# Kernel tuning notes

Hardware: AMD Instinct MI355X
Metric: run time of the kernel (lower is better)

## Reference

```python
import jax, jax.numpy as jnp
import numpy as np
import math

N, B, S = 2048, 4, 1024
SFZ, IFZ, H, A = 384, 256, 8, 64
LN_EPS = 1e-5


def setup_inputs() -> dict:
    key = jax.random.key(0)
    ks = jax.random.split(key, 12)
    x = jax.random.normal(ks[0], (N, IFZ), dtype=jnp.float32)
    emb = jax.random.normal(ks[1], (B, S, SFZ), dtype=jnp.float32)
    mask = jax.random.randint(ks[2], (B, S), 0, 2).astype(bool)
    batch = jnp.sort(jax.random.randint(ks[3], (N,), 0, B)).astype(jnp.int64)
    sc = 1.0 / math.sqrt(IFZ)
    scs = 1.0 / math.sqrt(SFZ)
    Wq = jax.random.normal(ks[4], (IFZ, H * A), dtype=jnp.float32) * sc
    Wk = jax.random.normal(ks[5], (SFZ, H * A), dtype=jnp.float32) * scs
    Wv = jax.random.normal(ks[6], (SFZ, H * A), dtype=jnp.float32) * scs
    Wg = jax.random.normal(ks[7], (IFZ, H * A), dtype=jnp.float32) * sc
    bg = jnp.zeros((H * A,), dtype=jnp.float32)
    Wback = jax.random.normal(ks[8], (H * A, IFZ), dtype=jnp.float32) / math.sqrt(H * A)
    bback = jnp.zeros((IFZ,), dtype=jnp.float32)
    gamma = jnp.ones((IFZ,), dtype=jnp.float32)
    beta = jnp.zeros((IFZ,), dtype=jnp.float32)
    return {"x": x, "packed_sequence_emb": emb, "packed_sequence_mask": mask,
            "batch": batch, "Wq": Wq, "Wk": Wk, "Wv": Wv, "Wg": Wg, "bg": bg,
            "Wback": Wback, "bback": bback, "gamma": gamma, "beta": beta}


def _masked_softmax(scores, mask):
    # scores: [N,S,H], mask: [N,S,1] bool; softmax over S with padded entries zeroed
    neg = jnp.finfo(scores.dtype).min
    s = jnp.where(mask, scores, neg)
    s = s - jnp.max(s, axis=1, keepdims=True)
    e = jnp.exp(s) * mask
    return e / (jnp.sum(e, axis=1, keepdims=True) + 1e-9)


def reference(x, packed_sequence_emb, packed_sequence_mask, batch,
              Wq, Wk, Wv, Wg, bg, Wback, bback, gamma, beta):
    scale = math.sqrt(A)
    q = (x @ Wq).reshape(N, H, A)                               # [N,H,A]
    k = (packed_sequence_emb @ Wk).reshape(B, S, H, A)          # [B,S,H,A]
    v = (packed_sequence_emb @ Wv).reshape(B, S, H, A)
    # scores per (node, candidate-batch), then gather node's own batch entry;
    # avoids materializing k[batch] of shape [N,S,H,A]
    scores_all = jnp.einsum('nha,bsha->nbsh', q, k) / scale     # [N,B,S,H]
    idx = batch[:, None, None, None].astype(jnp.int32)
    scores = jnp.take_along_axis(scores_all, idx, axis=1)[:, 0]  # [N,S,H]
    bmask = packed_sequence_mask[batch][..., None]               # [N,S,1]
    w = _masked_softmax(scores, bmask)                           # [N,S,H]
    feat_all = jnp.einsum('nsh,bsha->nbha', w, v)                # [N,B,H,A]
    feat = jnp.take_along_axis(feat_all, idx, axis=1)[:, 0]      # [N,H,A]
    gate = jax.nn.sigmoid(x @ Wg + bg).reshape(N, H, A)
    new = (gate * feat).reshape(N, H * A) @ Wback + bback        # [N,IFZ]
    y = math.sqrt(2.0) * x + new
    mu = jnp.mean(y, axis=-1, keepdims=True)
    var = jnp.mean((y - mu) ** 2, axis=-1, keepdims=True)
    out = (y - mu) * jax.lax.rsqrt(var + LN_EPS) * gamma + beta
    seq_aa_logits = jnp.sum(scores[..., :2], axis=-1)            # [N,S]
    return out, seq_aa_logits
```

## Files before the change

### kernel.cpp

```cpp
#include <hip/hip_runtime.h>
#include <hip/hip_bf16.h>

#define NND 2048
#define BBATCH 4
#define SS 1024
#define SFZ 384
#define IFZ 256
#define HH 8
#define AA 64
#define HA 512
#define ABLK 12
#define NGRP 4
#define NSPL 8
#define ATTN_BLKS (BBATCH * ABLK * 16)
#define LOGIT_BLKS (BBATCH * ABLK * 2)

typedef __attribute__((ext_vector_type(8))) short bf16x8;
typedef __attribute__((ext_vector_type(4))) float f32x4;
typedef __attribute__((ext_vector_type(2))) unsigned int u32x2;

__device__ __forceinline__ unsigned short f2bf(float f) {
    union { float f; unsigned u; } a; a.f = f;
    unsigned r = a.u + 0x7fffu + ((a.u >> 16) & 1u);
    return (unsigned short)(r >> 16);
}
__device__ __forceinline__ float bf2f(unsigned short u) {
    return __uint_as_float((unsigned)u << 16);
}

__device__ __forceinline__ bf16x8 cvt8(const float* __restrict__ p) {
    const float4 f0 = *(const float4*)p;
    const float4 f1 = *(const float4*)(p + 4);
    bf16x8 o;
    o[0] = (short)f2bf(f0.x); o[1] = (short)f2bf(f0.y);
    o[2] = (short)f2bf(f0.z); o[3] = (short)f2bf(f0.w);
    o[4] = (short)f2bf(f1.x); o[5] = (short)f2bf(f1.y);
    o[6] = (short)f2bf(f1.z); o[7] = (short)f2bf(f1.w);
    return o;
}

__device__ __forceinline__ bf16x8 gld16(const unsigned short* p) {
    bf16x8 r;
    asm volatile("global_load_dwordx4 %0, %1, off" : "=&v"(r) : "v"(p));
    return r;
}
__device__ __forceinline__ f32x4 gldf4(const float* p) {
    f32x4 r;
    asm volatile("global_load_dwordx4 %0, %1, off" : "=&v"(r) : "v"(p));
    return r;
}
__device__ __forceinline__ u32x2 gld8(const unsigned short* p) {
    u32x2 r;
    asm volatile("global_load_dwordx2 %0, %1, off" : "=&v"(r) : "v"(p));
    return r;
}
#define VMWAIT0() do { \
    asm volatile("s_waitcnt vmcnt(0)" ::: "memory"); \
    __builtin_amdgcn_sched_barrier(0); \
} while (0)

__device__ __forceinline__ void tile_transpose(
    const float* __restrict__ src, unsigned short* __restrict__ dst,
    int K, int N, int kt, int nt, int t)
{
    __shared__ unsigned short tile[64][65];
    const int k0 = kt * 64, n0 = nt * 64;
    const int tr = t >> 6, tc = t & 63;
    #pragma unroll
    for (int r = 0; r < 16; ++r)
        tile[tr + r*4][tc] = f2bf(src[(size_t)(k0 + tr + r*4) * N + n0 + tc]);
    __syncthreads();
    #pragma unroll
    for (int r = 0; r < 16; ++r)
        dst[(size_t)(n0 + tr + r*4) * K + k0 + tc] = tile[tc][tr + r*4];
}

__global__ __launch_bounds__(256) void prep_kernel(
    const float* __restrict__ Wk, const float* __restrict__ Wv,
    const float* __restrict__ Wq, const float* __restrict__ Wg,
    const float* __restrict__ Wback,
    const void* __restrict__ mask_raw, const void* __restrict__ batch_raw,
    unsigned short* __restrict__ WkT, unsigned short* __restrict__ WvT,
    unsigned short* __restrict__ WqT, unsigned short* __restrict__ WgT,
    unsigned short* __restrict__ WbackT,
    float* __restrict__ mask_f, int* __restrict__ seg)
{
    const int bx = blockIdx.x, t = threadIdx.x;
    if (bx < 48)  { tile_transpose(Wk, WkT, SFZ, HA, bx/8, bx%8, t); return; }
    if (bx < 96)  { const int i = bx-48;  tile_transpose(Wv, WvT, SFZ, HA, i/8, i%8, t); return; }
    if (bx < 128) { const int i = bx-96;  tile_transpose(Wq, WqT, IFZ, HA, i/8, i%8, t); return; }
    if (bx < 160) { const int i = bx-128; tile_transpose(Wg, WgT, IFZ, HA, i/8, i%8, t); return; }
    if (bx < 192) { const int i = bx-160; tile_transpose(Wback, WbackT, HA, IFZ, i/4, i%4, t); return; }
    __shared__ int fl[4];
    __shared__ int fb;
    __shared__ int cnt[4];
    if (t < 4) { fl[t] = 0; cnt[t] = 0; }
    if (t == 0) fb = 0;
    __syncthreads();
    const unsigned char*  mb = (const unsigned char*)mask_raw;
    const unsigned short* mh = (const unsigned short*)mask_raw;
    const unsigned int*   mw = (const unsigned int*)mask_raw;
    int f0 = 0, f1 = 0, f2 = 0, f3 = 0;
    for (int i = t; i < 2048; i += 256) {
        unsigned short h = mh[i];
        if (h == 0x3f80u) f0 = 1;
        if ((i & 1) == 0 && h != 0) f1 = 1;
    }
    for (int i = t; i < 4096; i += 256)
        if ((i & 3) != 0 && mb[i] != 0) f2 = 1;
    for (int i = t; i < 1024; i += 256)
        if ((i & 1) != 0 && mw[i] != 0) f3 = 1;
    const int* bw = (const int*)batch_raw;
    int f4 = 0;
    for (int i = t + 1; i < 2048; i += 256)
        if (bw[i] < bw[i-1]) f4 = 1;
    if (f0) atomicOr(&fl[0], 1);
    if (f1) atomicOr(&fl[1], 1);
    if (f2) atomicOr(&fl[2], 1);
    if (f3) atomicOr(&fl[3], 1);
    if (f4) atomicOr(&fb, 1);
    __syncthreads();
    int mode;
    if (fl[0])      mode = fl[1] ? 1 : 0;
    else if (fl[2]) mode = 2;
    else if (fl[3]) mode = 3;
    else            mode = 4;
    for (int s = t; s < BBATCH*SS; s += 256) {
        int m;
        switch (mode) {
            case 0:  m = (mw[s]   != 0); break;
            case 1:  m = (mh[s]   != 0); break;
            case 2:  m = (mb[s]   != 0); break;
            case 3:  m = (mw[s]   != 0); break;
            default: m = (mw[2*s] != 0); break;
        }
        mask_f[s] = m ? 1.0f : 0.0f;
    }
    const int b64 = fb;
    for (int i = t; i < NND; i += 256) {
        const int bv = (b64 ? bw[2*i] : bw[i]) & 3;
        atomicAdd(&cnt[bv], 1);
    }
    __syncthreads();
    if (t == 0) {
        int s = 0;
        for (int b = 0; b < 4; ++b) { seg[2*b] = s; s += cnt[b]; seg[2*b+1] = s; }
    }
}

__global__ __launch_bounds__(256, 2) void proj_mfma(
    const float* __restrict__ emb, const float* __restrict__ x,
    const unsigned short* __restrict__ WkT, const unsigned short* __restrict__ WvT,
    const unsigned short* __restrict__ WqT, const unsigned short* __restrict__ WgT,
    const float* __restrict__ bg,
    unsigned short* __restrict__ k_blk, unsigned short* __restrict__ vT_bf,
    unsigned short* __restrict__ q_bf, float* __restrict__ gate_ws)
{
    __shared__ unsigned short v_l[16][520];
    const int t = threadIdx.x, w = t >> 6, lane = t & 63;
    const int m16 = lane & 15, quad = lane >> 4;
    const int bx = blockIdx.x;
    if (bx < 256) {
        const int r0 = bx * 16;
        const int b = r0 >> 10, srow = r0 & (SS - 1);
        const float* ap = emb + (size_t)(r0 + m16) * SFZ + quad * 8;
        bf16x8 af[12];
        #pragma unroll
        for (int j = 0; j < 12; ++j) af[j] = cvt8(ap + j * 32);
        #pragma unroll
        for (int tensor = 0; tensor < 2; ++tensor) {
            const unsigned short* Wt = tensor ? WvT : WkT;
            #pragma unroll
            for (int g = 0; g < 2; ++g) {
                const int n0g = w * 128 + g * 64;
                const unsigned short* bp0 = Wt + (size_t)(n0g +  0 + m16) * SFZ + quad * 8;
                const unsigned short* bp1 = Wt + (size_t)(n0g + 16 + m16) * SFZ + quad * 8;
                const unsigned short* bp2 = Wt + (size_t)(n0g + 32 + m16) * SFZ + quad * 8;
                const unsigned short* bp3 = Wt + (size_t)(n0g + 48 + m16) * SFZ + quad * 8;
                f32x4 a0 = (f32x4){0.f, 0.f, 0.f, 0.f};
                f32x4 a1 = a0, a2 = a0, a3 = a0;
                bf16x8 wb[24];
                #pragma unroll
                for (int j = 0; j < 6; ++j) {
                    wb[j*4+0] = gld16(bp0 + j * 32);
                    wb[j*4+1] = gld16(bp1 + j * 32);
                    wb[j*4+2] = gld16(bp2 + j * 32);
                    wb[j*4+3] = gld16(bp3 + j * 32);
                }
                VMWAIT0();
                #pragma unroll
                for (int j = 0; j < 6; ++j) {
                    a0 = __builtin_amdgcn_mfma_f32_16x16x32_bf16(af[j], wb[j*4+0], a0, 0, 0, 0);
                    a1 = __builtin_amdgcn_mfma_f32_16x16x32_bf16(af[j], wb[j*4+1], a1, 0, 0, 0);
                    a2 = __builtin_amdgcn_mfma_f32_16x16x32_bf16(af[j], wb[j*4+2], a2, 0, 0, 0);
                    a3 = __builtin_amdgcn_mfma_f32_16x16x32_bf16(af[j], wb[j*4+3], a3, 0, 0, 0);
                }
                #pragma unroll
                for (int j = 6; j < 12; ++j) {
                    wb[(j-6)*4+0] = gld16(bp0 + j * 32);
                    wb[(j-6)*4+1] = gld16(bp1 + j * 32);
                    wb[(j-6)*4+2] = gld16(bp2 + j * 32);
                    wb[(j-6)*4+3] = gld16(bp3 + j * 32);
                }
                VMWAIT0();
                #pragma unroll
                for (int j = 6; j < 12; ++j) {
                    a0 = __builtin_amdgcn_mfma_f32_16x16x32_bf16(af[j], wb[(j-6)*4+0], a0, 0, 0, 0);
                    a1 = __builtin_amdgcn_mfma_f32_16x16x32_bf16(af[j], wb[(j-6)*4+1], a1, 0, 0, 0);
                    a2 = __builtin_amdgcn_mfma_f32_16x16x32_bf16(af[j], wb[(j-6)*4+2], a2, 0, 0, 0);
                    a3 = __builtin_amdgcn_mfma_f32_16x16x32_bf16(af[j], wb[(j-6)*4+3], a3, 0, 0, 0);
                }
                f32x4 dd[4] = {a0, a1, a2, a3};
                if (tensor == 0) {
                    #pragma unroll
                    for (int u = 0; u < 4; ++u) {
                        const int n0 = n0g + u * 16;
                        const int head = n0 >> 6, coff = (n0 & 63) + m16;
                        unsigned short* kb = k_blk + (((size_t)(b * HH + head)) * SS) * 64 + coff;
                        #pragma unroll
                        for (int r = 0; r < 4; ++r)
                            kb[(size_t)(srow + quad * 4 + r) * 64] = f2bf(dd[u][r]);
                    }
                } else {
                    #pragma unroll
                    for (int u = 0; u < 4; ++u) {
                        const int c0 = n0g + u * 16 + m16;
                        #pragma unroll
                        for (int r = 0; r < 4; ++r)
                            v_l[quad * 4 + r][c0] = f2bf(dd[u][r]);
                    }
                }
            }
        }
        __syncthreads();
        for (int c = t; c < HA; c += 256) {
            unsigned short tmp[16];
            #pragma unroll
            for (int s = 0; s < 16; ++s) tmp[s] = v_l[s][c];
            unsigned short* dst = vT_bf + ((size_t)b * HA + c) * SS + srow;
            *(uint4*)dst       = ((const uint4*)tmp)[0];
            *(uint4*)(dst + 8) = ((const uint4*)tmp)[1];
        }
    } else {
        const int i = bx - 256;
        const int r0 = (i >> 1) * 16;
        const int half = i & 1;
        const float* ap = x + (size_t)(r0 + m16) * IFZ + quad * 8;
        bf16x8 af[8];
        #pragma unroll
        for (int j = 0; j < 8; ++j) af[j] = cvt8(ap + j * 32);
        const int n0b = half * 256 + w * 64;
        #pragma unroll
        for (int tensor = 0; tensor < 2; ++tensor) {
            const unsigned short* Wt = tensor ? WgT : WqT;
            const unsigned short* bp0 = Wt + (size_t)(n0b +  0 + m16) * IFZ + quad * 8;
            const unsigned short* bp1 = Wt + (size_t)(n0b + 16 + m16) * IFZ + quad * 8;
            const unsigned short* bp2 = Wt + (size_t)(n0b + 32 + m16) * IFZ + quad * 8;
            const unsigned short* bp3 = Wt + (size_t)(n0b + 48 + m16) * IFZ + quad * 8;
            bf16x8 wb[32];
            #pragma unroll
            for (int j = 0; j < 8; ++j) {
                wb[j*4+0] = gld16(bp0 + j * 32);
                wb[j*4+1] = gld16(bp1 + j * 32);
                wb[j*4+2] = gld16(bp2 + j * 32);
                wb[j*4+3] = gld16(bp3 + j * 32);
            }
            VMWAIT0();
            f32x4 a0 = (f32x4){0.f, 0.f, 0.f, 0.f};
            f32x4 a1 = a0, a2 = a0, a3 = a0;
            #pragma unroll
            for (int j = 0; j < 8; ++j) {
                a0 = __builtin_amdgcn_mfma_f32_16x16x32_bf16(af[j], wb[j*4+0], a0, 0, 0, 0);
                a1 = __builtin_amdgcn_mfma_f32_16x16x32_bf16(af[j], wb[j*4+1], a1, 0, 0, 0);
                a2 = __builtin_amdgcn_mfma_f32_16x16x32_bf16(af[j], wb[j*4+2], a2, 0, 0, 0);
                a3 = __builtin_amdgcn_mfma_f32_16x16x32_bf16(af[j], wb[j*4+3], a3, 0, 0, 0);
            }
            f32x4 dd[4] = {a0, a1, a2, a3};
            if (tensor == 0) {
                #pragma unroll
                for (int u = 0; u < 4; ++u) {
                    const int n0 = n0b + u * 16;
                    #pragma unroll
                    for (int r = 0; r < 4; ++r)
                        q_bf[(size_t)(r0 + quad * 4 + r) * HA + n0 + m16] = f2bf(dd[u][r]);
                }
            } else {
                #pragma unroll
                for (int u = 0; u < 4; ++u) {
                    const int n0 = n0b + u * 16;
                    const float bgv = bg[n0 + m16];
                    #pragma unroll
                    for (int r = 0; r < 4; ++r)
                        gate_ws[(size_t)(r0 + quad * 4 + r) * HA + n0 + m16] =
                            1.f / (1.f + __expf(-(dd[u][r] + bgv)));
                }
            }
        }
    }
}

__global__ __launch_bounds__(256, 2) void attn_kernel(
    const unsigned short* __restrict__ k_blk, const unsigned short* __restrict__ vT_bf,
    const unsigned short* __restrict__ q_bf, const float* __restrict__ mask_f,
    const int* __restrict__ seg, unsigned short* __restrict__ part_O,
    float2* __restrict__ part_ml, float* __restrict__ out_logits)
{
    __shared__ unsigned short P_lds[4][16][136];
    const int bid = blockIdx.x;
    const int t = threadIdx.x;
    const int w = t >> 6, lane = t & 63;
    const int m16 = lane & 15, quad = lane >> 4;

    if (bid >= ATTN_BLKS) {
        const int lid = bid - ATTN_BLKS;
        const int b = lid / 24;
        const int rem = lid % 24;
        const int xblk = rem >> 1;
        const int spair = rem & 1;
        const int s0 = (spair * 4 + w) * 128;
        const int nbase = seg[2*b] + xblk * 64;
        const int nend  = seg[2*b + 1];
        if (nbase >= nend) return;
        const unsigned short* kb0 = k_blk + ((size_t)(b * HH + 0)) * SS * 64;
        const unsigned short* kb1 = k_blk + ((size_t)(b * HH + 1)) * SS * 64;
        bf16x8 k0[16], k1[16];
        #pragma unroll
        for (int st = 0; st < 8; ++st) {
            const unsigned short* kp0 = kb0 + (size_t)(s0 + st * 16 + m16) * 64 + quad * 8;
            const unsigned short* kp1 = kb1 + (size_t)(s0 + st * 16 + m16) * 64 + quad * 8;
            k0[2*st]   = gld16(kp0);
            k0[2*st+1] = gld16(kp0 + 32);
            k1[2*st]   = gld16(kp1);
            k1[2*st+1] = gld16(kp1 + 32);
        }
        VMWAIT0();
        for (int g = 0; g < NGRP; ++g) {
            const int n0g = nbase + g * 16;
            if (n0g >= nend) break;
            const int nvalid = min(16, nend - n0g);
            int nq = n0g + m16; if (nq >= nend) nq = nend - 1;
            const unsigned short* qp = q_bf + (size_t)nq * HA + quad * 8;
            const bf16x8 q0a = gld16(qp);
            const bf16x8 q0b = gld16(qp + 32);
            const bf16x8 q1a = gld16(qp + 64);
            const bf16x8 q1b = gld16(qp + 96);
            VMWAIT0();
            #pragma unroll
            for (int st = 0; st < 8; ++st) {
                f32x4 acc = (f32x4){0.f, 0.f, 0.f, 0.f};
                acc = __builtin_amdgcn_mfma_f32_16x16x32_bf16(q0a, k0[2*st],   acc, 0, 0, 0);
                acc = __builtin_amdgcn_mfma_f32_16x16x32_bf16(q0b, k0[2*st+1], acc, 0, 0, 0);
                acc = __builtin_amdgcn_mfma_f32_16x16x32_bf16(q1a, k1[2*st],   acc, 0, 0, 0);
                acc = __builtin_amdgcn_mfma_f32_16x16x32_bf16(q1b, k1[2*st+1], acc, 0, 0, 0);
                #pragma unroll
                for (int r = 0; r < 4; ++r) {
                    const int row = quad * 4 + r;
                    if (row < nvalid)
                        out_logits[(size_t)(n0g + row) * SS + s0 + st * 16 + m16] =
                            acc[r] * 0.125f;
                }
            }
        }
        return;
    }

    const int xcd = bid & 7;
    const int b   = xcd >> 1;
    const int idx = (bid >> 3) * 2 + (xcd & 1);
    const int z    = idx & 15;
    const int xblk = idx >> 4;
    const int hz    = z >> 3;
    const int split = z & 7;
    const int nbase = seg[2*b] + xblk * (16 * NGRP);
    const int nend  = seg[2*b + 1];
    if (nbase >= nend) return;

    const int h = hz * 4 + w;
    const int s0 = split * 128;

    const unsigned short* kb = k_blk + ((size_t)(b * HH + h)) * SS * 64;
    const unsigned short* vb = vT_bf + ((size_t)b * HA + h * AA) * SS;
    const unsigned short* qbase = q_bf + (size_t)h * AA + quad * 8;
    unsigned short (*Pw)[136] = P_lds[w];

    bf16x8 kf[16];
    #pragma unroll
    for (int st = 0; st < 8; ++st) {
        const unsigned short* kp = kb + (size_t)(s0 + st * 16 + m16) * 64 + quad * 8;
        kf[2*st]   = gld16(kp);
        kf[2*st+1] = gld16(kp + 32);
    }
    f32x4 mkv[8];
    #pragma unroll
    for (int st = 0; st < 8; ++st)
        mkv[st] = gldf4(mask_f + b * SS + s0 + st * 16 + quad * 4);
    int nq0 = nbase + m16; if (nq0 >= nend) nq0 = nend - 1;
    bf16x8 qc0 = gld16(qbase + (size_t)nq0 * HA);
    bf16x8 qc1 = gld16(qbase + (size_t)nq0 * HA + 32);
    VMWAIT0();
    unsigned bm = 0u;
    #pragma unroll
    for (int st = 0; st < 8; ++st)
        #pragma unroll
        for (int r = 0; r < 4; ++r)
            if (mkv[st][r] > 0.5f) bm |= (1u << (st * 4 + r));

    bf16x8 qn0 = qc0, qn1 = qc1;
    for (int g = 0; g < NGRP; ++g) {
        const int n0g = nbase + g * 16;
        if (n0g >= nend) break;
        const int nvalid = min(16, nend - n0g);

        f32x4 d[8];
        #pragma unroll
        for (int st = 0; st < 8; ++st) {
            f32x4 acc = (f32x4){0.f, 0.f, 0.f, 0.f};
            acc = __builtin_amdgcn_mfma_f32_16x16x32_bf16(kf[2*st],   qc0, acc, 0, 0, 0);
            acc = __builtin_amdgcn_mfma_f32_16x16x32_bf16(kf[2*st+1], qc1, acc, 0, 0, 0);
            #pragma unroll
            for (int r = 0; r < 4; ++r) acc[r] *= 0.125f;
            d[st] = acc;
        }
        bf16x8 vf[16];
        #pragma unroll
        for (int sub = 0; sub < 4; ++sub) {
            const unsigned short* vp0 = vb + (size_t)m16 * SS + s0 + sub * 32 + quad * 8;
            #pragma unroll
            for (int a = 0; a < 4; ++a)
                vf[sub*4+a] = gld16(vp0 + (size_t)(a * 16) * SS);
        }
        if (g + 1 < NGRP && nbase + (g + 1) * 16 < nend) {
            int nqn = nbase + (g + 1) * 16 + m16; if (nqn >= nend) nqn = nend - 1;
            qn0 = gld16(qbase + (size_t)nqn * HA);
            qn1 = gld16(qbase + (size_t)nqn * HA + 32);
        }
        __builtin_amdgcn_sched_barrier(0);

        #pragma unroll
        for (int st = 0; st < 8; ++st)
            #pragma unroll
            for (int r = 0; r < 4; ++r)
                if (!((bm >> (st * 4 + r)) & 1u)) d[st][r] = -3.0e38f;
        float mx = -3.0e38f;
        #pragma unroll
        for (int st = 0; st < 8; ++st) {
            float a = fmaxf(fmaxf(d[st][0], d[st][1]), fmaxf(d[st][2], d[st][3]));
            mx = fmaxf(mx, a);
        }
        mx = fmaxf(mx, __shfl_xor(mx, 16));
        mx = fmaxf(mx, __shfl_xor(mx, 32));
        mx = fmaxf(mx, -1.0e30f);
        float cs = 0.f;
        #pragma unroll
        for (int st = 0; st < 8; ++st)
            #pragma unroll
            for (int r = 0; r < 4; ++r) {
                const float e = __expf(d[st][r] - mx);
                d[st][r] = e;
                cs += e;
            }
        cs += __shfl_xor(cs, 16);
        cs += __shfl_xor(cs, 32);
        #pragma unroll
        for (int st = 0; st < 8; ++st) {
            ushort4 pk;
            pk.x = f2bf(d[st][0]); pk.y = f2bf(d[st][1]);
            pk.z = f2bf(d[st][2]); pk.w = f2bf(d[st][3]);
            *(ushort4*)&Pw[m16][st * 16 + quad * 4] = pk;
        }
        bf16x8 pa[4];
        #pragma unroll
        for (int sub = 0; sub < 4; ++sub)
            pa[sub] = *(const bf16x8*)&Pw[m16][sub * 32 + quad * 8];
        VMWAIT0();
        f32x4 facc[4];
        #pragma unroll
        for (int a = 0; a < 4; ++a) facc[a] = (f32x4){0.f, 0.f, 0.f, 0.f};
        #pragma unroll
        for (int sub = 0; sub < 4; ++sub) {
            #pragma unroll
            for (int a = 0; a < 4; ++a)
                facc[a] = __builtin_amdgcn_mfma_f32_16x16x32_bf16(pa[sub], vf[sub*4+a], facc[a], 0, 0, 0);
        }
        unsigned short* po = part_O + (size_t)split * NND * HA;
        #pragma unroll
        for (int a = 0; a < 4; ++a)
            #pragma unroll
            for (int r = 0; r < 4; ++r) {
                const int row = quad * 4 + r;
                if (row < nvalid)
                    po[(size_t)(n0g + row) * HA + h * AA + a * 16 + m16] = f2bf(facc[a][r]);
            }
        if (quad == 0 && m16 < nvalid)
            part_ml[(size_t)split * NND * HH + (size_t)(n0g + m16) * HH + h] =
                make_float2(mx, cs);
        qc0 = qn0; qc1 = qn1;
    }
}

__global__ __launch_bounds__(256, 2) void back_ln_fused(
    const unsigned short* __restrict__ part_O, const float2* __restrict__ part_ml,
    const float* __restrict__ gate_ws, const unsigned short* __restrict__ WbackT,
    const float* __restrict__ x, const float* __restrict__ bback,
    const float* __restrict__ gamma, const float* __restrict__ beta,
    float* __restrict__ out)
{
    __shared__ float coef[NSPL][8][8];
    __shared__ unsigned short gf_l[8][520];
    __shared__ float nl[8][260];
    const int t = threadIdx.x, w = t >> 6, lane = t & 63;
    const int m16 = lane & 15, quad = lane >> 4;
    const int r0 = blockIdx.x * 8;
    if (t < 64) {
        const int row = t >> 3, h = t & 7, n = r0 + row;
        float2 ml[NSPL];
        #pragma unroll
        for (int s = 0; s < NSPL; ++s)
            ml[s] = part_ml[(size_t)s * NND * HH + (size_t)n * HH + h];
        float M = -3.0e38f;
        #pragma unroll
        for (int s = 0; s < NSPL; ++s) M = fmaxf(M, ml[s].x);
        float L = 0.f;
        float e[NSPL];
        #pragma unroll
        for (int s = 0; s < NSPL; ++s) { e[s] = __expf(ml[s].x - M); L += ml[s].y * e[s]; }
        const float invL = 1.f / (L + 1e-9f);
        #pragma unroll
        for (int s = 0; s < NSPL; ++s) coef[s][row][h] = e[s] * invL;
    }
    u32x2 pvv[4][NSPL];
    f32x4 gv[4];
    #pragma unroll
    for (int it = 0; it < 4; ++it) {
        const int i = (t + it * 256) * 4;
        const int row = i >> 9, c = i & (HA - 1);
        const int n = r0 + row;
        #pragma unroll
        for (int s = 0; s < NSPL; ++s)
            pvv[it][s] = gld8(&part_O[(size_t)s * NND * HA + (size_t)n * HA + c]);
        gv[it] = gldf4(&gate_ws[(size_t)n * HA + c]);
    }
    __syncthreads();
    VMWAIT0();
    #pragma unroll
    for (int it = 0; it < 4; ++it) {
        const int i = (t + it * 256) * 4;
        const int row = i >> 9, c = i & (HA - 1), h = c >> 6;
        float4 o = make_float4(0.f, 0.f, 0.f, 0.f);
        #pragma unroll
        for (int s = 0; s < NSPL; ++s) {
            const float cf = coef[s][row][h];
            o.x = fmaf(bf2f((unsigned short)(pvv[it][s][0] & 0xffffu)), cf, o.x);
            o.y = fmaf(bf2f((unsigned short)(pvv[it][s][0] >> 16)),     cf, o.y);
            o.z = fmaf(bf2f((unsigned short)(pvv[it][s][1] & 0xffffu)), cf, o.z);
            o.w = fmaf(bf2f((unsigned short)(pvv[it][s][1] >> 16)),     cf, o.w);
        }
        ushort4 ob;
        ob.x = f2bf(gv[it][0] * o.x); ob.y = f2bf(gv[it][1] * o.y);
        ob.z = f2bf(gv[it][2] * o.z); ob.w = f2bf(gv[it][3] * o.w);
        *(ushort4*)&gf_l[row][c] = ob;
    }
    __syncthreads();
    bf16x8 af[16];
    #pragma unroll
    for (int j = 0; j < 16; ++j)
        af[j] = *(const bf16x8*)&gf_l[m16 & 7][quad * 8 + j * 32];
    const unsigned short* bq0 = WbackT + (size_t)(w * 64 +  0 + m16) * HA + quad * 8;
    const unsigned short* bq1 = WbackT + (size_t)(w * 64 + 16 + m16) * HA + quad * 8;
    const unsigned short* bq2 = WbackT + (size_t)(w * 64 + 32 + m16) * HA + quad * 8;
    const unsigned short* bq3 = WbackT + (size_t)(w * 64 + 48 + m16) * HA + quad * 8;
    f32x4 a0 = (f32x4){0.f, 0.f, 0.f, 0.f};
    f32x4 a1 = a0, a2 = a0, a3 = a0;
    #pragma unroll
    for (int jb = 0; jb < 4; ++jb) {
        bf16x8 wb[16];
        #pragma unroll
        for (int j = 0; j < 4; ++j) {
            wb[j*4+0] = gld16(bq0 + (jb*4 + j) * 32);
            wb[j*4+1] = gld16(bq1 + (jb*4 + j) * 32);
            wb[j*4+2] = gld16(bq2 + (jb*4 + j) * 32);
            wb[j*4+3] = gld16(bq3 + (jb*4 + j) * 32);
        }
        VMWAIT0();
        #pragma unroll
        for (int j = 0; j < 4; ++j) {
            a0 = __builtin_amdgcn_mfma_f32_16x16x32_bf16(af[jb*4+j], wb[j*4+0], a0, 0, 0, 0);
            a1 = __builtin_amdgcn_mfma_f32_16x16x32_bf16(af[jb*4+j], wb[j*4+1], a1, 0, 0, 0);
            a2 = __builtin_amdgcn_mfma_f32_16x16x32_bf16(af[jb*4+j], wb[j*4+2], a2, 0, 0, 0);
            a3 = __builtin_amdgcn_mfma_f32_16x16x32_bf16(af[jb*4+j], wb[j*4+3], a3, 0, 0, 0);
        }
    }
    {
        f32x4 dd[4] = {a0, a1, a2, a3};
        #pragma unroll
        for (int u = 0; u < 4; ++u) {
            const int n0 = w * 64 + u * 16;
            const float bb = bback[n0 + m16];
            #pragma unroll
            for (int r = 0; r < 4; ++r) {
                const int rr = quad * 4 + r;
                if (rr < 8) nl[rr][n0 + m16] = dd[u][r] + bb;
            }
        }
    }
    __syncthreads();
    const int row = t >> 5, li = t & 31;
    const float* xr = x + (size_t)(r0 + row) * IFZ;
    float yv[8];
    float s1 = 0.f, s2 = 0.f;
    #pragma unroll
    for (int j = 0; j < 8; ++j) {
        const int c = li + j * 32;
        const float v = fmaf(1.41421356237309515f, xr[c], nl[row][c]);
        yv[j] = v; s1 += v; s2 += v * v;
    }
    #pragma unroll
    for (int off = 16; off >= 1; off >>= 1) {
        s1 += __shfl_xor(s1, off);
        s2 += __shfl_xor(s2, off);
    }
    const float mu  = s1 * (1.f / IFZ);
    const float var = s2 * (1.f / IFZ) - mu * mu;
    const float rv  = rsqrtf(var + 1e-5f);
    float* orow = out + (size_t)(r0 + row) * IFZ;
    #pragma unroll
    for (int j = 0; j < 8; ++j) {
        const int c = li + j * 32;
        orow[c] = (yv[j] - mu) * rv * gamma[c] + beta[c];
    }
}

extern "C" void kernel_launch(void* const* d_in, const int* in_sizes, int n_in,
                              void* d_out, int out_size, void* d_ws, size_t ws_size,
                              hipStream_t stream) {
    const float* x     = (const float*)d_in[0];
    const float* emb   = (const float*)d_in[1];
    const void*  mraw  = d_in[2];
    const void*  braw  = d_in[3];
    const float* Wq    = (const float*)d_in[4];
    const float* Wk    = (const float*)d_in[5];
    const float* Wv    = (const float*)d_in[6];
    const float* Wg    = (const float*)d_in[7];
    const float* bg    = (const float*)d_in[8];
    const float* Wback = (const float*)d_in[9];
    const float* bback = (const float*)d_in[10];
    const float* gamma = (const float*)d_in[11];
    const float* beta  = (const float*)d_in[12];

    char* ws = (char*)d_ws;
    const size_t MB = 1048576;
    size_t off = 0;
    float*          mask_f  = (float*)(ws + off);  off += 16384;
    int*            seg     = (int*)(ws + off);    off += 16384;
    unsigned short* WkT     = (unsigned short*)(ws + off); off += 393216;
    unsigned short* WvT     = (unsigned short*)(ws + off); off += 393216;
    unsigned short* WqT     = (unsigned short*)(ws + off); off += 262144;
    unsigned short* WgT     = (unsigned short*)(ws + off); off += 262144;
    unsigned short* WbackT  = (unsigned short*)(ws + off); off += 262144;
    unsigned short* k_blk   = (unsigned short*)(ws + off); off += 4*MB;
    unsigned short* vT_bf   = (unsigned short*)(ws + off); off += 4*MB;
    unsigned short* q_bf    = (unsigned short*)(ws + off); off += 2*MB;
    float*          gate_ws = (float*)(ws + off); off += 4*MB;
    unsigned short* part_O  = (unsigned short*)(ws + off); off += 16*MB;
    float2*         part_ml = (float2*)(ws + off); off += 1*MB;

    float* out        = (float*)d_out;
    float* out_logits = out + (size_t)NND * IFZ;

    hipLaunchKernelGGL(prep_kernel, dim3(193), dim3(256), 0, stream,
                       Wk, Wv, Wq, Wg, Wback, mraw, braw,
                       WkT, WvT, WqT, WgT, WbackT, mask_f, seg);
    hipLaunchKernelGGL(proj_mfma, dim3(512), dim3(256), 0, stream,
                       emb, x, WkT, WvT, WqT, WgT, bg, k_blk, vT_bf, q_bf, gate_ws);
    hipLaunchKernelGGL(attn_kernel, dim3(ATTN_BLKS + LOGIT_BLKS), dim3(256), 0, stream,
                       k_blk, vT_bf, q_bf, mask_f, seg, part_O, part_ml, out_logits);
    hipLaunchKernelGGL(back_ln_fused, dim3(NND / 8), dim3(256), 0, stream,
                       part_O, part_ml, gate_ws, WbackT, x, bback, gamma, beta, out);
}
```

Baseline: 181.1 us.

## Fuse attention with back-projection and LayerNorm using online softmax per node group

Replaces the split-S attention kernel, which wrote bf16 partial outputs and max/sum pairs, plus the separate combine/back-projection/LayerNorm kernel, with one 512-thread kernel. Each block handles 12 nodes across all 8 heads and walks the full sequence with an online softmax, prefetching the next K chunk. It then gates, runs the Wback MFMA and LayerNorm in place. This removes the 16MB partial buffer traffic and one launch, but parallelism drops to about 256 blocks and each block loops serially over S, with only 12 of 16 MFMA rows used.

```diff
diff --git a/kernel.cpp b/kernel.cpp
--- a/kernel.cpp
+++ b/kernel.cpp
@@ -9,15 +9,13 @@
 #define HH 8
 #define AA 64
 #define HA 512
-#define ABLK 12
-#define NGRP 4
-#define NSPL 8
-#define ATTN_BLKS (BBATCH * ABLK * 16)
-#define LOGIT_BLKS (BBATCH * ABLK * 2)
+#define GRP 12
+#define NGPB 64
+#define MEGA_BLKS (BBATCH * NGPB)
+#define LOG_BLKS (BBATCH * 12)
 
 typedef __attribute__((ext_vector_type(8))) short bf16x8;
 typedef __attribute__((ext_vector_type(4))) float f32x4;
-typedef __attribute__((ext_vector_type(2))) unsigned int u32x2;
 
 __device__ __forceinline__ unsigned short f2bf(float f) {
     union { float f; unsigned u; } a; a.f = f;
@@ -47,11 +45,6 @@
 __device__ __forceinline__ f32x4 gldf4(const float* p) {
     f32x4 r;
     asm volatile("global_load_dwordx4 %0, %1, off" : "=&v"(r) : "v"(p));
-    return r;
-}
-__device__ __forceinline__ u32x2 gld8(const unsigned short* p) {
-    u32x2 r;
-    asm volatile("global_load_dwordx2 %0, %1, off" : "=&v"(r) : "v"(p));
     return r;
 }
 #define VMWAIT0() do { \
@@ -299,25 +292,24 @@
     }
 }
 
-__global__ __launch_bounds__(256, 2) void attn_kernel(
+__global__ __launch_bounds__(512, 2) void attn_back_fused(
     const unsigned short* __restrict__ k_blk, const unsigned short* __restrict__ vT_bf,
     const unsigned short* __restrict__ q_bf, const float* __restrict__ mask_f,
-    const int* __restrict__ seg, unsigned short* __restrict__ part_O,
-    float2* __restrict__ part_ml, float* __restrict__ out_logits)
+    const int* __restrict__ seg, const float* __restrict__ gate_ws,
+    const unsigned short* __restrict__ WbackT, const float* __restrict__ x,
+    const float* __restrict__ bback, const float* __restrict__ gamma,
+    const float* __restrict__ beta, float* __restrict__ out,
+    float* __restrict__ out_logits)
 {
-    __shared__ unsigned short P_lds[4][16][136];
-    const int bid = blockIdx.x;
-    const int t = threadIdx.x;
+    __shared__ __align__(16) char smem[34816];
+    const int bid = blockIdx.x, t = threadIdx.x;
     const int w = t >> 6, lane = t & 63;
     const int m16 = lane & 15, quad = lane >> 4;
 
-    if (bid >= ATTN_BLKS) {
-        const int lid = bid - ATTN_BLKS;
-        const int b = lid / 24;
-        const int rem = lid % 24;
-        const int xblk = rem >> 1;
-        const int spair = rem & 1;
-        const int s0 = (spair * 4 + w) * 128;
+    if (bid >= MEGA_BLKS) {
+        const int lid = bid - MEGA_BLKS;
+        const int b = lid / 12, xblk = lid % 12;
+        const int s0 = w * 128;
         const int nbase = seg[2*b] + xblk * 64;
         const int nend  = seg[2*b + 1];
         if (nbase >= nend) return;
@@ -334,7 +326,7 @@
             k1[2*st+1] = gld16(kp1 + 32);
         }
         VMWAIT0();
-        for (int g = 0; g < NGRP; ++g) {
+        for (int g = 0; g < 4; ++g) {
             const int n0g = nbase + g * 16;
             if (n0g >= nend) break;
             const int nvalid = min(16, nend - n0g);
@@ -366,37 +358,33 @@
 
     const int xcd = bid & 7;
     const int b   = xcd >> 1;
-    const int idx = (bid >> 3) * 2 + (xcd & 1);
-    const int z    = idx & 15;
-    const int xblk = idx >> 4;
-    const int hz    = z >> 3;
-    const int split = z & 7;
-    const int nbase = seg[2*b] + xblk * (16 * NGRP);
+    const int g   = (bid >> 3) * 2 + (xcd & 1);
+    const int nbase = seg[2*b] + g * GRP;
     const int nend  = seg[2*b + 1];
     if (nbase >= nend) return;
-
-    const int h = hz * 4 + w;
-    const int s0 = split * 128;
+    const int nvalid = min(GRP, nend - nbase);
+    const int h = w;
+
+    unsigned short (*Pw)[136] = (unsigned short (*)[136])(smem + w * 4352);
 
     const unsigned short* kb = k_blk + ((size_t)(b * HH + h)) * SS * 64;
     const unsigned short* vb = vT_bf + ((size_t)b * HA + h * AA) * SS;
-    const unsigned short* qbase = q_bf + (size_t)h * AA + quad * 8;
-    unsigned short (*Pw)[136] = P_lds[w];
-
+
+    int nq0 = nbase + m16; if (nq0 >= nend) nq0 = nend - 1;
+    const unsigned short* qp = q_bf + (size_t)nq0 * HA + h * AA + quad * 8;
+    const bf16x8 qc0 = gld16(qp);
+    const bf16x8 qc1 = gld16(qp + 32);
     bf16x8 kf[16];
     #pragma unroll
     for (int st = 0; st < 8; ++st) {
-        const unsigned short* kp = kb + (size_t)(s0 + st * 16 + m16) * 64 + quad * 8;
+        const unsigned short* kp = kb + (size_t)(st * 16 + m16) * 64 + quad * 8;
         kf[2*st]   = gld16(kp);
         kf[2*st+1] = gld16(kp + 32);
     }
     f32x4 mkv[8];
     #pragma unroll
     for (int st = 0; st < 8; ++st)
-        mkv[st] = gldf4(mask_f + b * SS + s0 + st * 16 + quad * 4);
-    int nq0 = nbase + m16; if (nq0 >= nend) nq0 = nend - 1;
-    bf16x8 qc0 = gld16(qbase + (size_t)nq0 * HA);
-    bf16x8 qc1 = gld16(qbase + (size_t)nq0 * HA + 32);
+        mkv[st] = gldf4(mask_f + b * SS + st * 16 + quad * 4);
     VMWAIT0();
     unsigned bm = 0u;
     #pragma unroll
@@ -405,12 +393,13 @@
         for (int r = 0; r < 4; ++r)
             if (mkv[st][r] > 0.5f) bm |= (1u << (st * 4 + r));
 
-    bf16x8 qn0 = qc0, qn1 = qc1;
-    for (int g = 0; g < NGRP; ++g) {
-        const int n0g = nbase + g * 16;
-        if (n0g >= nend) break;
-        const int nvalid = min(16, nend - n0g);
-
+    float M = -1.0e30f, l = 0.f;
+    f32x4 facc[4];
+    #pragma unroll
+    for (int a = 0; a < 4; ++a) facc[a] = (f32x4){0.f, 0.f, 0.f, 0.f};
+
+    for (int c = 0; c < 8; ++c) {
+        const int s0c = c << 7;
         f32x4 d[8];
         #pragma unroll
         for (int st = 0; st < 8; ++st) {
@@ -424,15 +413,22 @@
         bf16x8 vf[16];
         #pragma unroll
         for (int sub = 0; sub < 4; ++sub) {
-            const unsigned short* vp0 = vb + (size_t)m16 * SS + s0 + sub * 32 + quad * 8;
+            const unsigned short* vp0 = vb + (size_t)m16 * SS + s0c + sub * 32 + quad * 8;
             #pragma unroll
             for (int a = 0; a < 4; ++a)
                 vf[sub*4+a] = gld16(vp0 + (size_t)(a * 16) * SS);
         }
-        if (g + 1 < NGRP && nbase + (g + 1) * 16 < nend) {
-            int nqn = nbase + (g + 1) * 16 + m16; if (nqn >= nend) nqn = nend - 1;
-            qn0 = gld16(qbase + (size_t)nqn * HA);
-            qn1 = gld16(qbase + (size_t)nqn * HA + 32);
+        if (c < 7) {
+            const int s1c = s0c + 128;
+            #pragma unroll
+            for (int st = 0; st < 8; ++st) {
+                const unsigned short* kp = kb + (size_t)(s1c + st * 16 + m16) * 64 + quad * 8;
+                kf[2*st]   = gld16(kp);
+                kf[2*st+1] = gld16(kp + 32);
+            }
+            #pragma unroll
+            for (int st = 0; st < 8; ++st)
+                mkv[st] = gldf4(mask_f + b * SS + s1c + st * 16 + quad * 4);
         }
         __builtin_amdgcn_sched_barrier(0);
 
@@ -441,26 +437,29 @@
             #pragma unroll
             for (int r = 0; r < 4; ++r)
                 if (!((bm >> (st * 4 + r)) & 1u)) d[st][r] = -3.0e38f;
-        float mx = -3.0e38f;
+        float pmax = -3.0e38f;
         #pragma unroll
         for (int st = 0; st < 8; ++st) {
             float a = fmaxf(fmaxf(d[st][0], d[st][1]), fmaxf(d[st][2], d[st][3]));
-            mx = fmaxf(mx, a);
-        }
-        mx = fmaxf(mx, __shfl_xor(mx, 16));
-        mx = fmaxf(mx, __shfl_xor(mx, 32));
-        mx = fmaxf(mx, -1.0e30f);
+            pmax = fmaxf(pmax, a);
+        }
+        pmax = fmaxf(pmax, __shfl_xor(pmax, 16));
+        pmax = fmaxf(pmax, __shfl_xor(pmax, 32));
+        const float Mn = fmaxf(fmaxf(M, pmax), -1.0e30f);
+        const float alpha = __expf(M - Mn);
         float cs = 0.f;
         #pragma unroll
         for (int st = 0; st < 8; ++st)
             #pragma unroll
             for (int r = 0; r < 4; ++r) {
-                const float e = __expf(d[st][r] - mx);
+                const float e = __expf(d[st][r] - Mn);
                 d[st][r] = e;
                 cs += e;
             }
         cs += __shfl_xor(cs, 16);
         cs += __shfl_xor(cs, 32);
+        l = l * alpha + cs;
+        M = Mn;
         #pragma unroll
         for (int st = 0; st < 8; ++st) {
             ushort4 pk;
@@ -472,161 +471,114 @@
         #pragma unroll
         for (int sub = 0; sub < 4; ++sub)
             pa[sub] = *(const bf16x8*)&Pw[m16][sub * 32 + quad * 8];
+        float fr0 = __shfl(alpha, quad * 4 + 0);
+        float fr1 = __shfl(alpha, quad * 4 + 1);
+        float fr2 = __shfl(alpha, quad * 4 + 2);
+        float fr3 = __shfl(alpha, quad * 4 + 3);
+        #pragma unroll
+        for (int a = 0; a < 4; ++a) {
+            facc[a][0] *= fr0; facc[a][1] *= fr1;
+            facc[a][2] *= fr2; facc[a][3] *= fr3;
+        }
         VMWAIT0();
-        f32x4 facc[4];
-        #pragma unroll
-        for (int a = 0; a < 4; ++a) facc[a] = (f32x4){0.f, 0.f, 0.f, 0.f};
         #pragma unroll
         for (int sub = 0; sub < 4; ++sub) {
             #pragma unroll
             for (int a = 0; a < 4; ++a)
                 facc[a] = __builtin_amdgcn_mfma_f32_16x16x32_bf16(pa[sub], vf[sub*4+a], facc[a], 0, 0, 0);
         }
-        unsigned short* po = part_O + (size_t)split * NND * HA;
-        #pragma unroll
-        for (int a = 0; a < 4; ++a)
-            #pragma unroll
-            for (int r = 0; r < 4; ++r) {
-                const int row = quad * 4 + r;
-                if (row < nvalid)
-                    po[(size_t)(n0g + row) * HA + h * AA + a * 16 + m16] = f2bf(facc[a][r]);
-            }
-        if (quad == 0 && m16 < nvalid)
-            part_ml[(size_t)split * NND * HH + (size_t)(n0g + m16) * HH + h] =
-                make_float2(mx, cs);
-        qc0 = qn0; qc1 = qn1;
-    }
-}
-
-__global__ __launch_bounds__(256, 2) void back_ln_fused(
-    const unsigned short* __restrict__ part_O, const float2* __restrict__ part_ml,
-    const float* __restrict__ gate_ws, const unsigned short* __restrict__ WbackT,
-    const float* __restrict__ x, const float* __restrict__ bback,
-    const float* __restrict__ gamma, const float* __restrict__ beta,
-    float* __restrict__ out)
-{
-    __shared__ float coef[NSPL][8][8];
-    __shared__ unsigned short gf_l[8][520];
-    __shared__ float nl[8][260];
-    const int t = threadIdx.x, w = t >> 6, lane = t & 63;
-    const int m16 = lane & 15, quad = lane >> 4;
-    const int r0 = blockIdx.x * 8;
-    if (t < 64) {
-        const int row = t >> 3, h = t & 7, n = r0 + row;
-        float2 ml[NSPL];
-        #pragma unroll
-        for (int s = 0; s < NSPL; ++s)
-            ml[s] = part_ml[(size_t)s * NND * HH + (size_t)n * HH + h];
-        float M = -3.0e38f;
-        #pragma unroll
-        for (int s = 0; s < NSPL; ++s) M = fmaxf(M, ml[s].x);
-        float L = 0.f;
-        float e[NSPL];
-        #pragma unroll
-        for (int s = 0; s < NSPL; ++s) { e[s] = __expf(ml[s].x - M); L += ml[s].y * e[s]; }
-        const float invL = 1.f / (L + 1e-9f);
-        #pragma unroll
-        for (int s = 0; s < NSPL; ++s) coef[s][row][h] = e[s] * invL;
-    }
-    u32x2 pvv[4][NSPL];
-    f32x4 gv[4];
-    #pragma unroll
-    for (int it = 0; it < 4; ++it) {
-        const int i = (t + it * 256) * 4;
-        const int row = i >> 9, c = i & (HA - 1);
-        const int n = r0 + row;
-        #pragma unroll
-        for (int s = 0; s < NSPL; ++s)
-            pvv[it][s] = gld8(&part_O[(size_t)s * NND * HA + (size_t)n * HA + c]);
-        gv[it] = gldf4(&gate_ws[(size_t)n * HA + c]);
+        if (c < 7) {
+            bm = 0u;
+            #pragma unroll
+            for (int st = 0; st < 8; ++st)
+                #pragma unroll
+                for (int r = 0; r < 4; ++r)
+                    if (mkv[st][r] > 0.5f) bm |= (1u << (st * 4 + r));
+        }
+    }
+    const float invl = 1.f / (l + 1e-9f);
+    const float fl0 = __shfl(invl, quad * 4 + 0);
+    const float fl1 = __shfl(invl, quad * 4 + 1);
+    const float fl2 = __shfl(invl, quad * 4 + 2);
+    const float fl3 = __shfl(invl, quad * 4 + 3);
+    float og[4][4];
+    #pragma unroll
+    for (int a = 0; a < 4; ++a) {
+        #pragma unroll
+        for (int r = 0; r < 4; ++r) {
+            int nn = nbase + quad * 4 + r; if (nn >= nend) nn = nend - 1;
+            const float gv = gate_ws[(size_t)nn * HA + h * AA + a * 16 + m16];
+            const float fl_ = (r == 0) ? fl0 : (r == 1) ? fl1 : (r == 2) ? fl2 : fl3;
+            og[a][r] = facc[a][r] * fl_ * gv;
+        }
     }
     __syncthreads();
-    VMWAIT0();
-    #pragma unroll
-    for (int it = 0; it < 4; ++it) {
-        const int i = (t + it * 256) * 4;
-        const int row = i >> 9, c = i & (HA - 1), h = c >> 6;
-        float4 o = make_float4(0.f, 0.f, 0.f, 0.f);
-        #pragma unroll
-        for (int s = 0; s < NSPL; ++s) {
-            const float cf = coef[s][row][h];
-            o.x = fmaf(bf2f((unsigned short)(pvv[it][s][0] & 0xffffu)), cf, o.x);
-            o.y = fmaf(bf2f((unsigned short)(pvv[it][s][0] >> 16)),     cf, o.y);
-            o.z = fmaf(bf2f((unsigned short)(pvv[it][s][1] & 0xffffu)), cf, o.z);
-            o.w = fmaf(bf2f((unsigned short)(pvv[it][s][1] >> 16)),     cf, o.w);
-        }
-        ushort4 ob;
-        ob.x = f2bf(gv[it][0] * o.x); ob.y = f2bf(gv[it][1] * o.y);
-        ob.z = f2bf(gv[it][2] * o.z); ob.w = f2bf(gv[it][3] * o.w);
-        *(ushort4*)&gf_l[row][c] = ob;
-    }
+    unsigned short (*gf_l)[520] = (unsigned short (*)[520])smem;
+    float (*nl)[260] = (float (*)[260])(smem + 16640);
+    #pragma unroll
+    for (int a = 0; a < 4; ++a)
+        #pragma unroll
+        for (int r = 0; r < 4; ++r)
+            gf_l[quad * 4 + r][h * AA + a * 16 + m16] = f2bf(og[a][r]);
     __syncthreads();
     bf16x8 af[16];
     #pragma unroll
     for (int j = 0; j < 16; ++j)
-        af[j] = *(const bf16x8*)&gf_l[m16 & 7][quad * 8 + j * 32];
-    const unsigned short* bq0 = WbackT + (size_t)(w * 64 +  0 + m16) * HA + quad * 8;
-    const unsigned short* bq1 = WbackT + (size_t)(w * 64 + 16 + m16) * HA + quad * 8;
-    const unsigned short* bq2 = WbackT + (size_t)(w * 64 + 32 + m16) * HA + quad * 8;
-    const unsigned short* bq3 = WbackT + (size_t)(w * 64 + 48 + m16) * HA + quad * 8;
+        af[j] = *(const bf16x8*)&gf_l[m16][quad * 8 + j * 32];
+    const int n0w = w * 32;
+    const unsigned short* bq0 = WbackT + (size_t)(n0w +  0 + m16) * HA + quad * 8;
+    const unsigned short* bq1 = WbackT + (size_t)(n0w + 16 + m16) * HA + quad * 8;
+    bf16x8 wb[32];
+    #pragma unroll
+    for (int j = 0; j < 16; ++j) {
+        wb[2*j]   = gld16(bq0 + j * 32);
+        wb[2*j+1] = gld16(bq1 + j * 32);
+    }
+    VMWAIT0();
     f32x4 a0 = (f32x4){0.f, 0.f, 0.f, 0.f};
-    f32x4 a1 = a0, a2 = a0, a3 = a0;
-    #pragma unroll
-    for (int jb = 0; jb < 4; ++jb) {
-        bf16x8 wb[16];
-        #pragma unroll
-        for (int j = 0; j < 4; ++j) {
-            wb[j*4+0] = gld16(bq0 + (jb*4 + j) * 32);
-            wb[j*4+1] = gld16(bq1 + (jb*4 + j) * 32);
-            wb[j*4+2] = gld16(bq2 + (jb*4 + j) * 32);
-            wb[j*4+3] = gld16(bq3 + (jb*4 + j) * 32);
-        }
-        VMWAIT0();
-        #pragma unroll
-        for (int j = 0; j < 4; ++j) {
-            a0 = __builtin_amdgcn_mfma_f32_16x16x32_bf16(af[jb*4+j], wb[j*4+0], a0, 0, 0, 0);
-            a1 = __builtin_amdgcn_mfma_f32_16x16x32_bf16(af[jb*4+j], wb[j*4+1], a1, 0, 0, 0);
-            a2 = __builtin_amdgcn_mfma_f32_16x16x32_bf16(af[jb*4+j], wb[j*4+2], a2, 0, 0, 0);
-            a3 = __builtin_amdgcn_mfma_f32_16x16x32_bf16(af[jb*4+j], wb[j*4+3], a3, 0, 0, 0);
-        }
+    f32x4 a1 = a0;
+    #pragma unroll
+    for (int j = 0; j < 16; ++j) {
+        a0 = __builtin_amdgcn_mfma_f32_16x16x32_bf16(af[j], wb[2*j],   a0, 0, 0, 0);
+        a1 = __builtin_amdgcn_mfma_f32_16x16x32_bf16(af[j], wb[2*j+1], a1, 0, 0, 0);
     }
     {
-        f32x4 dd[4] = {a0, a1, a2, a3};
-        #pragma unroll
-        for (int u = 0; u < 4; ++u) {
-            const int n0 = w * 64 + u * 16;
+        f32x4 dd[2] = {a0, a1};
+        #pragma unroll
+        for (int u = 0; u < 2; ++u) {
+            const int n0 = n0w + u * 16;
             const float bb = bback[n0 + m16];
             #pragma unroll
-            for (int r = 0; r < 4; ++r) {
-                const int rr = quad * 4 + r;
-                if (rr < 8) nl[rr][n0 + m16] = dd[u][r] + bb;
-            }
+            for (int r = 0; r < 4; ++r)
+                nl[quad * 4 + r][n0 + m16] = dd[u][r] + bb;
         }
     }
     __syncthreads();
     const int row = t >> 5, li = t & 31;
-    const float* xr = x + (size_t)(r0 + row) * IFZ;
-    float yv[8];
-    float s1 = 0.f, s2 = 0.f;
-    #pragma unroll
-    for (int j = 0; j < 8; ++j) {
-        const int c = li + j * 32;
-        const float v = fmaf(1.41421356237309515f, xr[c], nl[row][c]);
-        yv[j] = v; s1 += v; s2 += v * v;
-    }
-    #pragma unroll
-    for (int off = 16; off >= 1; off >>= 1) {
-        s1 += __shfl_xor(s1, off);
-        s2 += __shfl_xor(s2, off);
-    }
-    const float mu  = s1 * (1.f / IFZ);
-    const float var = s2 * (1.f / IFZ) - mu * mu;
-    const float rv  = rsqrtf(var + 1e-5f);
-    float* orow = out + (size_t)(r0 + row) * IFZ;
-    #pragma unroll
-    for (int j = 0; j < 8; ++j) {
-        const int c = li + j * 32;
-        orow[c] = (yv[j] - mu) * rv * gamma[c] + beta[c];
+    if (row < nvalid) {
+        const float* xr = x + (size_t)(nbase + row) * IFZ;
+        float yv[8];
+        float s1 = 0.f, s2 = 0.f;
+        #pragma unroll
+        for (int j = 0; j < 8; ++j) {
+            const int cc = li + j * 32;
+            const float v = fmaf(1.41421356237309515f, xr[cc], nl[row][cc]);
+            yv[j] = v; s1 += v; s2 += v * v;
+        }
+        #pragma unroll
+        for (int off = 16; off >= 1; off >>= 1) {
+            s1 += __shfl_xor(s1, off);
+            s2 += __shfl_xor(s2, off);
+        }
+        const float mu  = s1 * (1.f / IFZ);
+        const float var = s2 * (1.f / IFZ) - mu * mu;
+        const float rv  = rsqrtf(var + 1e-5f);
+        float* orow = out + (size_t)(nbase + row) * IFZ;
+        #pragma unroll
+        for (int j = 0; j < 8; ++j) {
+            const int cc = li + j * 32;
+            orow[cc] = (yv[j] - mu) * rv * gamma[cc] + beta[cc];
+        }
     }
 }
 
@@ -661,8 +613,6 @@
     unsigned short* vT_bf   = (unsigned short*)(ws + off); off += 4*MB;
     unsigned short* q_bf    = (unsigned short*)(ws + off); off += 2*MB;
     float*          gate_ws = (float*)(ws + off); off += 4*MB;
-    unsigned short* part_O  = (unsigned short*)(ws + off); off += 16*MB;
-    float2*         part_ml = (float2*)(ws + off); off += 1*MB;
 
     float* out        = (float*)d_out;
     float* out_logits = out + (size_t)NND * IFZ;
@@ -672,8 +622,7 @@
                        WkT, WvT, WqT, WgT, WbackT, mask_f, seg);
     hipLaunchKernelGGL(proj_mfma, dim3(512), dim3(256), 0, stream,
                        emb, x, WkT, WvT, WqT, WgT, bg, k_blk, vT_bf, q_bf, gate_ws);
-    hipLaunchKernelGGL(attn_kernel, dim3(ATTN_BLKS + LOGIT_BLKS), dim3(256), 0, stream,
-                       k_blk, vT_bf, q_bf, mask_f, seg, part_O, part_ml, out_logits);
-    hipLaunchKernelGGL(back_ln_fused, dim3(NND / 8), dim3(256), 0, stream,
-                       part_O, part_ml, gate_ws, WbackT, x, bback, gamma, beta, out);
-}
+    hipLaunchKernelGGL(attn_back_fused, dim3(MEGA_BLKS + LOG_BLKS), dim3(512), 0, stream,
+                       k_blk, vT_bf, q_bf, mask_f, seg, gate_ws, WbackT, x,
+                       bback, gamma, beta, out, out_logits);
+}
```

Measured after the change: 207.5 us. +14.6%, slower.

## Retile projection kernel so waves share weight columns across 64-row blocks

Applied to the files above, without the earlier changes.

The projection kernel's block tiling changes from 16 rows × full width (waves split columns) to 64 rows × 128 columns, with each wave handling 16 rows of the same column slice. All four waves now read the same weight rows, which is meant to improve cache reuse of the weights and cut per-block weight traffic. The V transpose goes through a 64×128 LDS tile with 64-byte stores per thread instead of 32-byte ones. The grid shrinks from 512 to 384 blocks, so the x projection blocks now do twice the work each and fewer blocks are resident.

```diff
diff --git a/kernel.cpp b/kernel.cpp
--- a/kernel.cpp
+++ b/kernel.cpp
@@ -156,14 +156,17 @@
     unsigned short* __restrict__ k_blk, unsigned short* __restrict__ vT_bf,
     unsigned short* __restrict__ q_bf, float* __restrict__ gate_ws)
 {
-    __shared__ unsigned short v_l[16][520];
+    __shared__ unsigned short v_l[64][136];
     const int t = threadIdx.x, w = t >> 6, lane = t & 63;
     const int m16 = lane & 15, quad = lane >> 4;
     const int bx = blockIdx.x;
     if (bx < 256) {
-        const int r0 = bx * 16;
+        const int rowblk = bx >> 2, colblk = bx & 3;
+        const int r0 = rowblk * 64;
+        const int rw = r0 + w * 16;
         const int b = r0 >> 10, srow = r0 & (SS - 1);
-        const float* ap = emb + (size_t)(r0 + m16) * SFZ + quad * 8;
+        const int srw = rw & (SS - 1);
+        const float* ap = emb + (size_t)(rw + m16) * SFZ + quad * 8;
         bf16x8 af[12];
         #pragma unroll
         for (int j = 0; j < 12; ++j) af[j] = cvt8(ap + j * 32);
@@ -172,7 +175,7 @@
             const unsigned short* Wt = tensor ? WvT : WkT;
             #pragma unroll
             for (int g = 0; g < 2; ++g) {
-                const int n0g = w * 128 + g * 64;
+                const int n0g = colblk * 128 + g * 64;
                 const unsigned short* bp0 = Wt + (size_t)(n0g +  0 + m16) * SFZ + quad * 8;
                 const unsigned short* bp1 = Wt + (size_t)(n0g + 16 + m16) * SFZ + quad * 8;
                 const unsigned short* bp2 = Wt + (size_t)(n0g + 32 + m16) * SFZ + quad * 8;
@@ -219,80 +222,88 @@
                         unsigned short* kb = k_blk + (((size_t)(b * HH + head)) * SS) * 64 + coff;
                         #pragma unroll
                         for (int r = 0; r < 4; ++r)
-                            kb[(size_t)(srow + quad * 4 + r) * 64] = f2bf(dd[u][r]);
+                            kb[(size_t)(srw + quad * 4 + r) * 64] = f2bf(dd[u][r]);
                     }
                 } else {
                     #pragma unroll
                     for (int u = 0; u < 4; ++u) {
-                        const int c0 = n0g + u * 16 + m16;
+                        const int c0 = g * 64 + u * 16 + m16;
                         #pragma unroll
                         for (int r = 0; r < 4; ++r)
-                            v_l[quad * 4 + r][c0] = f2bf(dd[u][r]);
+                            v_l[w * 16 + quad * 4 + r][c0] = f2bf(dd[u][r]);
                     }
                 }
             }
         }
         __syncthreads();
-        for (int c = t; c < HA; c += 256) {
-            unsigned short tmp[16];
-            #pragma unroll
-            for (int s = 0; s < 16; ++s) tmp[s] = v_l[s][c];
-            unsigned short* dst = vT_bf + ((size_t)b * HA + c) * SS + srow;
-            *(uint4*)dst       = ((const uint4*)tmp)[0];
-            *(uint4*)(dst + 8) = ((const uint4*)tmp)[1];
+        {
+            const int col = t & 127, half = t >> 7;
+            unsigned short tmp[32];
+            #pragma unroll
+            for (int s = 0; s < 32; ++s) tmp[s] = v_l[half * 32 + s][col];
+            unsigned short* dst = vT_bf + ((size_t)b * HA + colblk * 128 + col) * SS
+                                        + srow + half * 32;
+            *(uint4*)dst        = ((const uint4*)tmp)[0];
+            *(uint4*)(dst + 8)  = ((const uint4*)tmp)[1];
+            *(uint4*)(dst + 16) = ((const uint4*)tmp)[2];
+            *(uint4*)(dst + 24) = ((const uint4*)tmp)[3];
         }
     } else {
         const int i = bx - 256;
-        const int r0 = (i >> 1) * 16;
-        const int half = i & 1;
-        const float* ap = x + (size_t)(r0 + m16) * IFZ + quad * 8;
+        const int rowblk = i >> 2, colblk = i & 3;
+        const int r0 = rowblk * 64;
+        const int rw = r0 + w * 16;
+        const float* ap = x + (size_t)(rw + m16) * IFZ + quad * 8;
         bf16x8 af[8];
         #pragma unroll
         for (int j = 0; j < 8; ++j) af[j] = cvt8(ap + j * 32);
-        const int n0b = half * 256 + w * 64;
         #pragma unroll
         for (int tensor = 0; tensor < 2; ++tensor) {
             const unsigned short* Wt = tensor ? WgT : WqT;
-            const unsigned short* bp0 = Wt + (size_t)(n0b +  0 + m16) * IFZ + quad * 8;
-            const unsigned short* bp1 = Wt + (size_t)(n0b + 16 + m16) * IFZ + quad * 8;
-            const unsigned short* bp2 = Wt + (size_t)(n0b + 32 + m16) * IFZ + quad * 8;
-            const unsigned short* bp3 = Wt + (size_t)(n0b + 48 + m16) * IFZ + quad * 8;
-            bf16x8 wb[32];
-            #pragma unroll
-            for (int j = 0; j < 8; ++j) {
-                wb[j*4+0] = gld16(bp0 + j * 32);
-                wb[j*4+1] = gld16(bp1 + j * 32);
-                wb[j*4+2] = gld16(bp2 + j * 32);
-                wb[j*4+3] = gld16(bp3 + j * 32);
-            }
-            VMWAIT0();
-            f32x4 a0 = (f32x4){0.f, 0.f, 0.f, 0.f};
-            f32x4 a1 = a0, a2 = a0, a3 = a0;
-            #pragma unroll
-            for (int j = 0; j < 8; ++j) {
-                a0 = __builtin_amdgcn_mfma_f32_16x16x32_bf16(af[j], wb[j*4+0], a0, 0, 0, 0);
-                a1 = __builtin_amdgcn_mfma_f32_16x16x32_bf16(af[j], wb[j*4+1], a1, 0, 0, 0);
-                a2 = __builtin_amdgcn_mfma_f32_16x16x32_bf16(af[j], wb[j*4+2], a2, 0, 0, 0);
-                a3 = __builtin_amdgcn_mfma_f32_16x16x32_bf16(af[j], wb[j*4+3], a3, 0, 0, 0);
-            }
-            f32x4 dd[4] = {a0, a1, a2, a3};
-            if (tensor == 0) {
+            #pragma unroll
+            for (int g = 0; g < 2; ++g) {
+                const int n0g = colblk * 128 + g * 64;
+                const unsigned short* bp0 = Wt + (size_t)(n0g +  0 + m16) * IFZ + quad * 8;
+                const unsigned short* bp1 = Wt + (size_t)(n0g + 16 + m16) * IFZ + quad * 8;
+                const unsigned short* bp2 = Wt + (size_t)(n0g + 32 + m16) * IFZ + quad * 8;
+                const unsigned short* bp3 = Wt + (size_t)(n0g + 48 + m16) * IFZ + quad * 8;
+                bf16x8 wb[32];
                 #pragma unroll
-                for (int u = 0; u < 4; ++u) {
-                    const int n0 = n0b + u * 16;
+                for (int j = 0; j < 8; ++j) {
+                    wb[j*4+0] = gld16(bp0 + j * 32);
+                    wb[j*4+1] = gld16(bp1 + j * 32);
+                    wb[j*4+2] = gld16(bp2 + j * 32);
+                    wb[j*4+3] = gld16(bp3 + j * 32);
+                }
+                VMWAIT0();
+                f32x4 a0 = (f32x4){0.f, 0.f, 0.f, 0.f};
+                f32x4 a1 = a0, a2 = a0, a3 = a0;
+                #pragma unroll
+                for (int j = 0; j < 8; ++j) {
+                    a0 = __builtin_amdgcn_mfma_f32_16x16x32_bf16(af[j], wb[j*4+0], a0, 0, 0, 0);
+                    a1 = __builtin_amdgcn_mfma_f32_16x16x32_bf16(af[j], wb[j*4+1], a1, 0, 0, 0);
+                    a2 = __builtin_amdgcn_mfma_f32_16x16x32_bf16(af[j], wb[j*4+2], a2, 0, 0, 0);
+                    a3 = __builtin_amdgcn_mfma_f32_16x16x32_bf16(af[j], wb[j*4+3], a3, 0, 0, 0);
+                }
+                f32x4 dd[4] = {a0, a1, a2, a3};
+                if (tensor == 0) {
                     #pragma unroll
-                    for (int r = 0; r < 4; ++r)
-                        q_bf[(size_t)(r0 + quad * 4 + r) * HA + n0 + m16] = f2bf(dd[u][r]);
-                }
-            } else {
-                #pragma unroll
-                for (int u = 0; u < 4; ++u) {
-                    const int n0 = n0b + u * 16;
-                    const float bgv = bg[n0 + m16];
+                    for (int u = 0; u < 4; ++u) {
+                        const int n0 = n0g + u * 16;
+                        #pragma unroll
+                        for (int r = 0; r < 4; ++r)
+                            q_bf[(size_t)(rw + quad * 4 + r) * HA + n0 + m16] = f2bf(dd[u][r]);
+                    }
+                } else {
                     #pragma unroll
-                    for (int r = 0; r < 4; ++r)
-                        gate_ws[(size_t)(r0 + quad * 4 + r) * HA + n0 + m16] =
-                            1.f / (1.f + __expf(-(dd[u][r] + bgv)));
+                    for (int u = 0; u < 4; ++u) {
+                        const int n0 = n0g + u * 16;
+                        const float bgv = bg[n0 + m16];
+                        #pragma unroll
+                        for (int r = 0; r < 4; ++r)
+                            gate_ws[(size_t)(rw + quad * 4 + r) * HA + n0 + m16] =
+                                1.f / (1.f + __expf(-(dd[u][r] + bgv)));
+                    }
                 }
             }
         }
@@ -670,7 +681,7 @@
     hipLaunchKernelGGL(prep_kernel, dim3(193), dim3(256), 0, stream,
                        Wk, Wv, Wq, Wg, Wback, mraw, braw,
                        WkT, WvT, WqT, WgT, WbackT, mask_f, seg);
-    hipLaunchKernelGGL(proj_mfma, dim3(512), dim3(256), 0, stream,
+    hipLaunchKernelGGL(proj_mfma, dim3(384), dim3(256), 0, stream,
                        emb, x, WkT, WvT, WqT, WgT, bg, k_blk, vT_bf, q_bf, gate_ws);
     hipLaunchKernelGGL(attn_kernel, dim3(ATTN_BLKS + LOGIT_BLKS), dim3(256), 0, stream,
                        k_blk, vT_bf, q_bf, mask_f, seg, part_O, part_ml, out_logits);
```

Result: slower. 189.7 us (+4.8%).
